# Kernel tuning notes

Hardware: AMD Instinct MI355X
Metric: run time of the kernel (lower is better)

The kernel has to match this reference:

```python
import jax, jax.numpy as jnp
import numpy as np
import math

B, S, D, H = 2, 2048, 1024, 16
DK = D // H

def setup_inputs() -> dict:
    key = jax.random.key(0)
    ks = jax.random.split(key, 12)
    std = 1.0 / math.sqrt(D)
    inp = {
        'query': jax.random.normal(ks[0], (B, S, D), jnp.float32),
        'key':   jax.random.normal(ks[1], (B, S, D), jnp.float32),
        'value': jax.random.normal(ks[2], (B, S, D), jnp.float32),
        'mask':  jnp.ones((B, 1, 1, S), dtype=bool),
        'wq': jax.random.normal(ks[3], (D, D), jnp.float32) * std,
        'bq': jnp.zeros((D,), jnp.float32),
        'wk': jax.random.normal(ks[4], (D, D), jnp.float32) * std,
        'bk': jnp.zeros((D,), jnp.float32),
        'wv': jax.random.normal(ks[5], (D, D), jnp.float32) * std,
        'bv': jnp.zeros((D,), jnp.float32),
        'wo': jax.random.normal(ks[6], (D, D), jnp.float32) * std,
        'bo': jnp.zeros((D,), jnp.float32),
    }
    return inp

def reference(query, key, value, mask, wq, bq, wk, bk, wv, bv, wo, bo):
    # torch.nn.Linear: y = x @ W^T + b
    def split_heads(x):  # [B,S,D] -> [B,H,S,DK]
        return x.reshape(B, -1, H, DK).transpose(0, 2, 1, 3)
    Q = split_heads(query @ wq.T + bq)
    K = split_heads(key @ wk.T + bk)
    V = split_heads(value @ wv.T + bv)
    scale = 1.0 / math.sqrt(DK)
    scores = jnp.einsum('bhtd,bhsd->bhts', Q, K * scale)  # [B,H,S,S]
    scores = jnp.where(mask, scores, -jnp.inf)
    attn = jax.nn.softmax(scores, axis=-1)
    # dropout p=0.0 (eval) -> identity
    context = jnp.einsum('bhts,bhsd->bhtd', attn, V)
    context = context.transpose(0, 2, 1, 3).reshape(B, -1, D)
    return context @ wo.T + bo
```

## Files before the change

kernel.cpp:

```cpp
#include <hip/hip_runtime.h>
#include <stdint.h>

#define SEQ 2048
#define NH  16

typedef __bf16 bf16x8 __attribute__((ext_vector_type(8)));
typedef float  f32x4  __attribute__((ext_vector_type(4)));

#if __has_builtin(__builtin_amdgcn_exp2f)
#define EXP2(x) __builtin_amdgcn_exp2f(x)
#else
#define EXP2(x) exp2f(x)
#endif

__device__ __forceinline__ unsigned short f2bf(float f) {
  union { float f; uint32_t u; } v; v.f = f;
  uint32_t r = v.u + 0x7fffu + ((v.u >> 16) & 1u);
  return (unsigned short)(r >> 16);
}

__device__ __forceinline__ void gll16(const void* g, void* l) {
  __builtin_amdgcn_global_load_lds((const __attribute__((address_space(1))) void*)g,
                                   (__attribute__((address_space(3))) void*)l, 16, 0, 0);
}

__device__ __forceinline__ f32x4 mfma16(bf16x8 a, bf16x8 b, f32x4 c) {
  return __builtin_amdgcn_mfma_f32_16x16x32_bf16(a, b, c, 0, 0, 0);
}

__global__ void cvt_bf16(const float* __restrict__ src, unsigned short* __restrict__ dst, int n4) {
  int i = blockIdx.x * blockDim.x + threadIdx.x;
  int st = gridDim.x * blockDim.x;
  for (; i < n4; i += st) {
    float4 v = ((const float4*)src)[i];
    union { unsigned short u[4]; uint2 q; } o;
    o.u[0] = f2bf(v.x); o.u[1] = f2bf(v.y); o.u[2] = f2bf(v.z); o.u[3] = f2bf(v.w);
    ((uint2*)dst)[i] = o.q;
  }
}

template<int MODE>
__global__ __launch_bounds__(256, 2) void gemm_bt(const unsigned short* __restrict__ A,
                                                  const unsigned short* __restrict__ W,
                                                  const float* __restrict__ bias,
                                                  void* __restrict__ outp, float scale) {
  __shared__ alignas(16) unsigned short Asm[64 * 64];
  __shared__ alignas(16) unsigned short Bsm[128 * 64];
  const int tid = threadIdx.x;
  const int l = tid & 63, w = tid >> 6;
  const int wr = w >> 1, wc = w & 1;
  const int lg = l >> 4, lo = l & 15;
  const int m0 = blockIdx.x * 64, n0 = blockIdx.y * 128;

  f32x4 acc[2][4] = {};

  for (int kt = 0; kt < 16; ++kt) {
    __syncthreads();
#pragma unroll
    for (int it = 0; it < 2; ++it) {
      int chunk = it * 256 + tid;
      int row = chunk >> 3, c = chunk & 7;
      const char* src = (const char*)A + (((size_t)(m0 + row) << 10) + (kt << 6)) * 2 + ((c ^ (row & 7)) << 4);
      gll16(src, (char*)Asm + ((it * 256 + (tid & ~63)) << 4));
    }
#pragma unroll
    for (int it = 0; it < 4; ++it) {
      int chunk = it * 256 + tid;
      int row = chunk >> 3, c = chunk & 7;
      const char* src = (const char*)W + (((size_t)(n0 + row) << 10) + (kt << 6)) * 2 + ((c ^ (row & 7)) << 4);
      gll16(src, (char*)Bsm + ((it * 256 + (tid & ~63)) << 4));
    }
    __syncthreads();
#pragma unroll
    for (int kf = 0; kf < 2; ++kf) {
      bf16x8 af[2], bfr[4];
#pragma unroll
      for (int mf = 0; mf < 2; ++mf) {
        int row = wr * 32 + mf * 16 + lo;
        int pos = (kf * 4 + lg) ^ (row & 7);
        af[mf] = *(const bf16x8*)((const char*)Asm + row * 128 + pos * 16);
      }
#pragma unroll
      for (int nf = 0; nf < 4; ++nf) {
        int row = wc * 64 + nf * 16 + lo;
        int pos = (kf * 4 + lg) ^ (row & 7);
        bfr[nf] = *(const bf16x8*)((const char*)Bsm + row * 128 + pos * 16);
      }
#pragma unroll
      for (int mf = 0; mf < 2; ++mf)
#pragma unroll
        for (int nf = 0; nf < 4; ++nf)
          acc[mf][nf] = mfma16(af[mf], bfr[nf], acc[mf][nf]);
    }
  }
#pragma unroll
  for (int mf = 0; mf < 2; ++mf)
#pragma unroll
    for (int nf = 0; nf < 4; ++nf) {
      int gcol = n0 + wc * 64 + nf * 16 + lo;
      float bv = bias[gcol];
#pragma unroll
      for (int r = 0; r < 4; ++r) {
        int grow = m0 + wr * 32 + mf * 16 + lg * 4 + r;
        float v = (acc[mf][nf][r] + bv) * scale;
        if (MODE == 2) {
          ((float*)outp)[((size_t)grow << 10) + gcol] = v;
        } else {
          int b = grow >> 11, s = grow & 2047, h = gcol >> 6, dk = gcol & 63;
          size_t idx;
          if (MODE == 0) idx = ((((size_t)((b << 4) + h) << 11) + s) << 6) + dk;
          else           idx = ((((size_t)((b << 4) + h) << 6) + dk) << 11) + s;
          ((unsigned short*)outp)[idx] = f2bf(v);
        }
      }
    }
}

__global__ __launch_bounds__(256, 2) void attn_kernel(const unsigned short* __restrict__ Qb,
                                                      const unsigned short* __restrict__ Kb,
                                                      const unsigned short* __restrict__ Vt,
                                                      unsigned short* __restrict__ ctx) {
  __shared__ alignas(16) unsigned short Ksm[64 * 64];
  __shared__ alignas(16) unsigned short Vsm[64 * 64];
  __shared__ alignas(16) unsigned short Psm[4 * 32 * 64];
  const int tid = threadIdx.x;
  const int l = tid & 63, w = tid >> 6;
  const int lg = l >> 4, lo = l & 15;
  const int bh = blockIdx.y;
  const unsigned short* Qp = Qb + (size_t)bh * SEQ * 64;
  const unsigned short* Kp = Kb + (size_t)bh * SEQ * 64;
  const unsigned short* Vp = Vt + (size_t)bh * 64 * SEQ;
  const int q0 = blockIdx.x * 128 + w * 32;

  bf16x8 qf[2][2];
#pragma unroll
  for (int mf = 0; mf < 2; ++mf)
#pragma unroll
    for (int kc = 0; kc < 2; ++kc)
      qf[mf][kc] = *(const bf16x8*)((const char*)Qp + (((size_t)(q0 + mf * 16 + lo)) << 7) + kc * 64 + lg * 16);

  f32x4 O[2][4] = {};
  float m_[2], l_[2];
  m_[0] = m_[1] = -1e30f;
  l_[0] = l_[1] = 0.f;

  for (int t = 0; t < SEQ / 64; ++t) {
    const int kv0 = t << 6;
    __syncthreads();
#pragma unroll
    for (int it = 0; it < 2; ++it) {
      int chunk = it * 256 + tid;
      int row = chunk >> 3, c = chunk & 7;
      const char* ksrc = (const char*)Kp + ((size_t)(kv0 + row) << 7) + ((c ^ (row & 7)) << 4);
      gll16(ksrc, (char*)Ksm + ((it * 256 + (tid & ~63)) << 4));
      const char* vsrc = (const char*)Vp + ((size_t)row << 12) + (kv0 << 1) + ((c ^ (row & 7)) << 4);
      gll16(vsrc, (char*)Vsm + ((it * 256 + (tid & ~63)) << 4));
    }
    __syncthreads();

    f32x4 sfr[4][2] = {};
#pragma unroll
    for (int kc = 0; kc < 2; ++kc) {
      bf16x8 kfr[4];
#pragma unroll
      for (int kvf = 0; kvf < 4; ++kvf) {
        int kv = kvf * 16 + lo;
        int pos = (kc * 4 + lg) ^ (kv & 7);
        kfr[kvf] = *(const bf16x8*)((const char*)Ksm + kv * 128 + pos * 16);
      }
#pragma unroll
      for (int kvf = 0; kvf < 4; ++kvf)
#pragma unroll
        for (int qfi = 0; qfi < 2; ++qfi)
          sfr[kvf][qfi] = mfma16(kfr[kvf], qf[qfi][kc], sfr[kvf][qfi]);
    }

    float tmx[2];
#pragma unroll
    for (int qfi = 0; qfi < 2; ++qfi) {
      float a0 = fmaxf(fmaxf(sfr[0][qfi][0], sfr[0][qfi][1]), fmaxf(sfr[0][qfi][2], sfr[0][qfi][3]));
      float a1 = fmaxf(fmaxf(sfr[1][qfi][0], sfr[1][qfi][1]), fmaxf(sfr[1][qfi][2], sfr[1][qfi][3]));
      float a2 = fmaxf(fmaxf(sfr[2][qfi][0], sfr[2][qfi][1]), fmaxf(sfr[2][qfi][2], sfr[2][qfi][3]));
      float a3 = fmaxf(fmaxf(sfr[3][qfi][0], sfr[3][qfi][1]), fmaxf(sfr[3][qfi][2], sfr[3][qfi][3]));
      float mx = fmaxf(fmaxf(a0, a1), fmaxf(a2, a3));
      mx = fmaxf(mx, __shfl_xor(mx, 16));
      mx = fmaxf(mx, __shfl_xor(mx, 32));
      tmx[qfi] = mx;
    }
    bool need = (tmx[0] > m_[0]) | (tmx[1] > m_[1]);
    if (__any((int)need)) {
      float facv[2];
#pragma unroll
      for (int qfi = 0; qfi < 2; ++qfi) {
        float mnew = fmaxf(m_[qfi], tmx[qfi]);
        facv[qfi] = EXP2(m_[qfi] - mnew);
        m_[qfi] = mnew;
        float ps = 0.f;
#pragma unroll
        for (int kvf = 0; kvf < 4; ++kvf)
#pragma unroll
          for (int r = 0; r < 4; ++r) {
            float p = EXP2(sfr[kvf][qfi][r] - mnew);
            sfr[kvf][qfi][r] = p;
            ps += p;
          }
        ps += __shfl_xor(ps, 16);
        ps += __shfl_xor(ps, 32);
        l_[qfi] = l_[qfi] * facv[qfi] + ps;
      }
#pragma unroll
      for (int mf = 0; mf < 2; ++mf)
#pragma unroll
        for (int r = 0; r < 4; ++r) {
          float fb = __shfl(facv[mf], lg * 4 + r);
#pragma unroll
          for (int dkf = 0; dkf < 4; ++dkf) O[mf][dkf][r] *= fb;
        }
    } else {
#pragma unroll
      for (int qfi = 0; qfi < 2; ++qfi) {
        float ps = 0.f;
#pragma unroll
        for (int kvf = 0; kvf < 4; ++kvf)
#pragma unroll
          for (int r = 0; r < 4; ++r) {
            float p = EXP2(sfr[kvf][qfi][r] - m_[qfi]);
            sfr[kvf][qfi][r] = p;
            ps += p;
          }
        ps += __shfl_xor(ps, 16);
        ps += __shfl_xor(ps, 32);
        l_[qfi] += ps;
      }
    }

#pragma unroll
    for (int qfi = 0; qfi < 2; ++qfi) {
      int ql = qfi * 16 + lo;
      int sw = ql & 7;
#pragma unroll
      for (int kvf = 0; kvf < 4; ++kvf) {
        union { __bf16 b[4]; unsigned long long u; } pk;
#pragma unroll
        for (int r = 0; r < 4; ++r) pk.b[r] = (__bf16)sfr[kvf][qfi][r];
        int g = kvf * 2 + (lg >> 1);
        *(unsigned long long*)((char*)Psm + w * 4096 + ql * 128 + ((g ^ sw) << 4) + ((lg & 1) << 3)) = pk.u;
      }
    }

    bf16x8 af[2][2];
#pragma unroll
    for (int mf = 0; mf < 2; ++mf)
#pragma unroll
      for (int kc = 0; kc < 2; ++kc) {
        int ql = mf * 16 + lo;
        int pos = (kc * 4 + lg) ^ (ql & 7);
        af[mf][kc] = *(const bf16x8*)((const char*)Psm + w * 4096 + ql * 128 + pos * 16);
      }
#pragma unroll
    for (int dkf = 0; dkf < 4; ++dkf) {
      bf16x8 bvf[2];
#pragma unroll
      for (int kc = 0; kc < 2; ++kc) {
        int dk = dkf * 16 + lo;
        int pos = (kc * 4 + lg) ^ (dk & 7);
        bvf[kc] = *(const bf16x8*)((const char*)Vsm + dk * 128 + pos * 16);
      }
#pragma unroll
      for (int mf = 0; mf < 2; ++mf) {
        O[mf][dkf] = mfma16(af[mf][0], bvf[0], O[mf][dkf]);
        O[mf][dkf] = mfma16(af[mf][1], bvf[1], O[mf][dkf]);
      }
    }
  }

  const int b = bh >> 4, h = bh & 15;
#pragma unroll
  for (int mf = 0; mf < 2; ++mf)
#pragma unroll
    for (int r = 0; r < 4; ++r) {
      float lr = __shfl(l_[mf], lg * 4 + r);
      float inv = 1.f / lr;
      int srow = q0 + mf * 16 + lg * 4 + r;
      size_t rowoff = ((size_t)(b * SEQ + srow) << 10) + h * 64;
#pragma unroll
      for (int dkf = 0; dkf < 4; ++dkf)
        ctx[rowoff + dkf * 16 + lo] = f2bf(O[mf][dkf][r] * inv);
    }
}

extern "C" void kernel_launch(void* const* d_in, const int* in_sizes, int n_in,
                              void* d_out, int out_size, void* d_ws, size_t ws_size,
                              hipStream_t stream) {
  const float* query = (const float*)d_in[0];
  const float* key_  = (const float*)d_in[1];
  const float* value = (const float*)d_in[2];
  const float* wq = (const float*)d_in[4];
  const float* bq = (const float*)d_in[5];
  const float* wk = (const float*)d_in[6];
  const float* bk = (const float*)d_in[7];
  const float* wv = (const float*)d_in[8];
  const float* bv = (const float*)d_in[9];
  const float* wo = (const float*)d_in[10];
  const float* bo = (const float*)d_in[11];
  float* out = (float*)d_out;

  char* ws = (char*)d_ws;
  unsigned short* xq  = (unsigned short*)(ws + 0);
  unsigned short* xk  = (unsigned short*)(ws + 8388608);
  unsigned short* xv  = (unsigned short*)(ws + 16777216);
  unsigned short* wqb = (unsigned short*)(ws + 25165824);
  unsigned short* wkb = (unsigned short*)(ws + 27262976);
  unsigned short* wvb = (unsigned short*)(ws + 29360128);
  unsigned short* wob = (unsigned short*)(ws + 31457280);
  unsigned short* Qb  = (unsigned short*)(ws + 33554432);
  unsigned short* Kb  = (unsigned short*)(ws + 41943040);
  unsigned short* Vb  = (unsigned short*)(ws + 50331648);
  unsigned short* ctx = (unsigned short*)(ws + 58720256);

  cvt_bf16<<<1024, 256, 0, stream>>>(query, xq, 1048576);
  cvt_bf16<<<1024, 256, 0, stream>>>(key_,  xk, 1048576);
  cvt_bf16<<<1024, 256, 0, stream>>>(value, xv, 1048576);
  cvt_bf16<<<512, 256, 0, stream>>>(wq, wqb, 262144);
  cvt_bf16<<<512, 256, 0, stream>>>(wk, wkb, 262144);
  cvt_bf16<<<512, 256, 0, stream>>>(wv, wvb, 262144);
  cvt_bf16<<<512, 256, 0, stream>>>(wo, wob, 262144);

  dim3 gg(64, 8);
  const float kscale = 0.125f * 1.44269504088896340736f;
  gemm_bt<0><<<gg, 256, 0, stream>>>(xq, wqb, bq, (void*)Qb, 1.0f);
  gemm_bt<0><<<gg, 256, 0, stream>>>(xk, wkb, bk, (void*)Kb, kscale);
  gemm_bt<1><<<gg, 256, 0, stream>>>(xv, wvb, bv, (void*)Vb, 1.0f);

  attn_kernel<<<dim3(16, 32), 256, 0, stream>>>(Qb, Kb, Vb, ctx);

  gemm_bt<2><<<gg, 256, 0, stream>>>(ctx, wob, bo, (void*)out, 1.0f);
}
```

Before: 157.3 us.

## Batch launches, double-buffer GEMM and attention loads, enlarge GEMM tiles

Merges the seven bf16 conversion launches into one grid and the three QKV projections into one batched GEMM launch. The GEMM moves to 128x128 tiles with a double-buffered LDS pipeline, overlapping the next tile's global-to-LDS copies with current MFMA work through explicit vmcnt waits. The attention kernel gets the same double-buffered K/V staging and a swizzled 1D block order for cache locality. This cuts launch overhead and exposed load latency, but the larger LDS footprint and accumulator register use may lower occupancy.

```diff
diff --git a/kernel.cpp b/kernel.cpp
--- a/kernel.cpp
+++ b/kernel.cpp
@@ -13,6 +13,11 @@
 #define EXP2(x) exp2f(x)
 #endif
 
+#define WAITV0 asm volatile("s_waitcnt vmcnt(0)" ::: "memory")
+#define WAITV4 asm volatile("s_waitcnt vmcnt(4)" ::: "memory")
+#define WAITV8 asm volatile("s_waitcnt vmcnt(8)" ::: "memory")
+#define SBAR() do { __builtin_amdgcn_sched_barrier(0); __builtin_amdgcn_s_barrier(); __builtin_amdgcn_sched_barrier(0); } while (0)
+
 __device__ __forceinline__ unsigned short f2bf(float f) {
   union { float f; uint32_t u; } v; v.f = f;
   uint32_t r = v.u + 0x7fffu + ((v.u >> 16) & 1u);
@@ -28,89 +33,133 @@
   return __builtin_amdgcn_mfma_f32_16x16x32_bf16(a, b, c, 0, 0, 0);
 }
 
-__global__ void cvt_bf16(const float* __restrict__ src, unsigned short* __restrict__ dst, int n4) {
-  int i = blockIdx.x * blockDim.x + threadIdx.x;
+struct CvtJobs {
+  const float* s[7];
+  unsigned short* d[7];
+  int n4[7];
+};
+
+__global__ void cvt_all(CvtJobs J) {
+  int j = blockIdx.y;
+  const float* __restrict__ s = J.s[j];
+  unsigned short* __restrict__ d = J.d[j];
+  int n4 = J.n4[j];
   int st = gridDim.x * blockDim.x;
-  for (; i < n4; i += st) {
-    float4 v = ((const float4*)src)[i];
+  for (int i = blockIdx.x * blockDim.x + threadIdx.x; i < n4; i += st) {
+    float4 v = ((const float4*)s)[i];
     union { unsigned short u[4]; uint2 q; } o;
     o.u[0] = f2bf(v.x); o.u[1] = f2bf(v.y); o.u[2] = f2bf(v.z); o.u[3] = f2bf(v.w);
-    ((uint2*)dst)[i] = o.q;
+    ((uint2*)d)[i] = o.q;
   }
 }
 
-template<int MODE>
-__global__ __launch_bounds__(256, 2) void gemm_bt(const unsigned short* __restrict__ A,
-                                                  const unsigned short* __restrict__ W,
-                                                  const float* __restrict__ bias,
-                                                  void* __restrict__ outp, float scale) {
-  __shared__ alignas(16) unsigned short Asm[64 * 64];
-  __shared__ alignas(16) unsigned short Bsm[128 * 64];
+struct GemmJobs {
+  const unsigned short* A[3];
+  const unsigned short* W[3];
+  const float* bias[3];
+  void* out[3];
+  float scale[3];
+  int mode[3];
+};
+
+__global__ __launch_bounds__(256, 2) void gemm128(GemmJobs J) {
+  __shared__ alignas(16) unsigned short Asm[2][128 * 64];
+  __shared__ alignas(16) unsigned short Bsm[2][128 * 64];
   const int tid = threadIdx.x;
   const int l = tid & 63, w = tid >> 6;
   const int wr = w >> 1, wc = w & 1;
   const int lg = l >> 4, lo = l & 15;
-  const int m0 = blockIdx.x * 64, n0 = blockIdx.y * 128;
-
-  f32x4 acc[2][4] = {};
+
+  const int nwg = gridDim.x;
+  const int id = blockIdx.x;
+  const int swz = (id & 7) * (nwg >> 3) + (id >> 3);
+  const int g = swz >> 8;
+  const int rem = swz & 255;
+  const int m0 = (rem & 31) * 128;
+  const int n0 = (rem >> 5) * 128;
+
+  const unsigned short* __restrict__ A = J.A[g];
+  const unsigned short* __restrict__ W = J.W[g];
+  const float* __restrict__ bias = J.bias[g];
+  const int mode = J.mode[g];
+  const float scale = J.scale[g];
+
+  f32x4 acc[4][4] = {};
+
+#define GSTAGE(b, kt)                                                                   \
+  do {                                                                                  \
+    _Pragma("unroll")                                                                   \
+    for (int it = 0; it < 4; ++it) {                                                    \
+      int chunk = it * 256 + tid;                                                       \
+      int row = chunk >> 3, c = chunk & 7;                                              \
+      const char* src = (const char*)A + (((size_t)(m0 + row) << 10) + ((kt) << 6)) * 2 \
+                        + ((c ^ (row & 7)) << 4);                                       \
+      gll16(src, (char*)Asm[b] + ((it * 256 + (tid & ~63)) << 4));                      \
+    }                                                                                   \
+    _Pragma("unroll")                                                                   \
+    for (int it = 0; it < 4; ++it) {                                                    \
+      int chunk = it * 256 + tid;                                                       \
+      int row = chunk >> 3, c = chunk & 7;                                              \
+      const char* src = (const char*)W + (((size_t)(n0 + row) << 10) + ((kt) << 6)) * 2 \
+                        + ((c ^ (row & 7)) << 4);                                       \
+      gll16(src, (char*)Bsm[b] + ((it * 256 + (tid & ~63)) << 4));                      \
+    }                                                                                   \
+  } while (0)
+
+  GSTAGE(0, 0);
 
   for (int kt = 0; kt < 16; ++kt) {
-    __syncthreads();
-#pragma unroll
-    for (int it = 0; it < 2; ++it) {
-      int chunk = it * 256 + tid;
-      int row = chunk >> 3, c = chunk & 7;
-      const char* src = (const char*)A + (((size_t)(m0 + row) << 10) + (kt << 6)) * 2 + ((c ^ (row & 7)) << 4);
-      gll16(src, (char*)Asm + ((it * 256 + (tid & ~63)) << 4));
-    }
-#pragma unroll
-    for (int it = 0; it < 4; ++it) {
-      int chunk = it * 256 + tid;
-      int row = chunk >> 3, c = chunk & 7;
-      const char* src = (const char*)W + (((size_t)(n0 + row) << 10) + (kt << 6)) * 2 + ((c ^ (row & 7)) << 4);
-      gll16(src, (char*)Bsm + ((it * 256 + (tid & ~63)) << 4));
-    }
-    __syncthreads();
+    const int cur = kt & 1;
+    if (kt < 15) {
+      GSTAGE(cur ^ 1, kt + 1);
+      WAITV8;
+    } else {
+      WAITV0;
+    }
+    SBAR();
 #pragma unroll
     for (int kf = 0; kf < 2; ++kf) {
-      bf16x8 af[2], bfr[4];
-#pragma unroll
-      for (int mf = 0; mf < 2; ++mf) {
-        int row = wr * 32 + mf * 16 + lo;
+      bf16x8 af[4], bfr[4];
+#pragma unroll
+      for (int mf = 0; mf < 4; ++mf) {
+        int row = wr * 64 + mf * 16 + lo;
         int pos = (kf * 4 + lg) ^ (row & 7);
-        af[mf] = *(const bf16x8*)((const char*)Asm + row * 128 + pos * 16);
+        af[mf] = *(const bf16x8*)((const char*)Asm[cur] + row * 128 + pos * 16);
       }
 #pragma unroll
       for (int nf = 0; nf < 4; ++nf) {
         int row = wc * 64 + nf * 16 + lo;
         int pos = (kf * 4 + lg) ^ (row & 7);
-        bfr[nf] = *(const bf16x8*)((const char*)Bsm + row * 128 + pos * 16);
-      }
-#pragma unroll
-      for (int mf = 0; mf < 2; ++mf)
+        bfr[nf] = *(const bf16x8*)((const char*)Bsm[cur] + row * 128 + pos * 16);
+      }
+#pragma unroll
+      for (int mf = 0; mf < 4; ++mf)
 #pragma unroll
         for (int nf = 0; nf < 4; ++nf)
           acc[mf][nf] = mfma16(af[mf], bfr[nf], acc[mf][nf]);
     }
+    SBAR();
   }
-#pragma unroll
-  for (int mf = 0; mf < 2; ++mf)
+#undef GSTAGE
+
+#pragma unroll
+  for (int mf = 0; mf < 4; ++mf)
 #pragma unroll
     for (int nf = 0; nf < 4; ++nf) {
       int gcol = n0 + wc * 64 + nf * 16 + lo;
       float bv = bias[gcol];
 #pragma unroll
       for (int r = 0; r < 4; ++r) {
-        int grow = m0 + wr * 32 + mf * 16 + lg * 4 + r;
+        int grow = m0 + wr * 64 + mf * 16 + lg * 4 + r;
         float v = (acc[mf][nf][r] + bv) * scale;
-        if (MODE == 2) {
-          ((float*)outp)[((size_t)grow << 10) + gcol] = v;
+        if (mode == 2) {
+          ((float*)J.out[g])[((size_t)grow << 10) + gcol] = v;
         } else {
           int b = grow >> 11, s = grow & 2047, h = gcol >> 6, dk = gcol & 63;
           size_t idx;
-          if (MODE == 0) idx = ((((size_t)((b << 4) + h) << 11) + s) << 6) + dk;
+          if (mode == 0) idx = ((((size_t)((b << 4) + h) << 11) + s) << 6) + dk;
           else           idx = ((((size_t)((b << 4) + h) << 6) + dk) << 11) + s;
-          ((unsigned short*)outp)[idx] = f2bf(v);
+          ((__bf16*)J.out[g])[idx] = (__bf16)v;
         }
       }
     }
@@ -120,17 +169,22 @@
                                                       const unsigned short* __restrict__ Kb,
                                                       const unsigned short* __restrict__ Vt,
                                                       unsigned short* __restrict__ ctx) {
-  __shared__ alignas(16) unsigned short Ksm[64 * 64];
-  __shared__ alignas(16) unsigned short Vsm[64 * 64];
+  __shared__ alignas(16) unsigned short Ksm[2][64 * 64];
+  __shared__ alignas(16) unsigned short Vsm[2][64 * 64];
   __shared__ alignas(16) unsigned short Psm[4 * 32 * 64];
   const int tid = threadIdx.x;
   const int l = tid & 63, w = tid >> 6;
   const int lg = l >> 4, lo = l & 15;
-  const int bh = blockIdx.y;
+
+  const int id = blockIdx.x;
+  const int swz = (id & 7) * 64 + (id >> 3);
+  const int bh = swz >> 4;
+  const int qt = swz & 15;
+
   const unsigned short* Qp = Qb + (size_t)bh * SEQ * 64;
   const unsigned short* Kp = Kb + (size_t)bh * SEQ * 64;
   const unsigned short* Vp = Vt + (size_t)bh * 64 * SEQ;
-  const int q0 = blockIdx.x * 128 + w * 32;
+  const int q0 = qt * 128 + w * 32;
 
   bf16x8 qf[2][2];
 #pragma unroll
@@ -138,25 +192,38 @@
 #pragma unroll
     for (int kc = 0; kc < 2; ++kc)
       qf[mf][kc] = *(const bf16x8*)((const char*)Qp + (((size_t)(q0 + mf * 16 + lo)) << 7) + kc * 64 + lg * 16);
+  WAITV0;
 
   f32x4 O[2][4] = {};
   float m_[2], l_[2];
   m_[0] = m_[1] = -1e30f;
   l_[0] = l_[1] = 0.f;
 
+#define ASTAGE(b, t)                                                                      \
+  do {                                                                                    \
+    const int kv0s = (t) << 6;                                                            \
+    _Pragma("unroll")                                                                     \
+    for (int it = 0; it < 2; ++it) {                                                      \
+      int chunk = it * 256 + tid;                                                         \
+      int row = chunk >> 3, c = chunk & 7;                                                \
+      const char* ksrc = (const char*)Kp + ((size_t)(kv0s + row) << 7) + ((c ^ (row & 7)) << 4); \
+      gll16(ksrc, (char*)Ksm[b] + ((it * 256 + (tid & ~63)) << 4));                       \
+      const char* vsrc = (const char*)Vp + ((size_t)row << 12) + (kv0s << 1) + ((c ^ (row & 7)) << 4); \
+      gll16(vsrc, (char*)Vsm[b] + ((it * 256 + (tid & ~63)) << 4));                       \
+    }                                                                                     \
+  } while (0)
+
+  ASTAGE(0, 0);
+
   for (int t = 0; t < SEQ / 64; ++t) {
-    const int kv0 = t << 6;
-    __syncthreads();
-#pragma unroll
-    for (int it = 0; it < 2; ++it) {
-      int chunk = it * 256 + tid;
-      int row = chunk >> 3, c = chunk & 7;
-      const char* ksrc = (const char*)Kp + ((size_t)(kv0 + row) << 7) + ((c ^ (row & 7)) << 4);
-      gll16(ksrc, (char*)Ksm + ((it * 256 + (tid & ~63)) << 4));
-      const char* vsrc = (const char*)Vp + ((size_t)row << 12) + (kv0 << 1) + ((c ^ (row & 7)) << 4);
-      gll16(vsrc, (char*)Vsm + ((it * 256 + (tid & ~63)) << 4));
-    }
-    __syncthreads();
+    const int cur = t & 1;
+    if (t < SEQ / 64 - 1) {
+      ASTAGE(cur ^ 1, t + 1);
+      WAITV4;
+    } else {
+      WAITV0;
+    }
+    SBAR();
 
     f32x4 sfr[4][2] = {};
 #pragma unroll
@@ -166,7 +233,7 @@
       for (int kvf = 0; kvf < 4; ++kvf) {
         int kv = kvf * 16 + lo;
         int pos = (kc * 4 + lg) ^ (kv & 7);
-        kfr[kvf] = *(const bf16x8*)((const char*)Ksm + kv * 128 + pos * 16);
+        kfr[kvf] = *(const bf16x8*)((const char*)Ksm[cur] + kv * 128 + pos * 16);
       }
 #pragma unroll
       for (int kvf = 0; kvf < 4; ++kvf)
@@ -264,7 +331,7 @@
       for (int kc = 0; kc < 2; ++kc) {
         int dk = dkf * 16 + lo;
         int pos = (kc * 4 + lg) ^ (dk & 7);
-        bvf[kc] = *(const bf16x8*)((const char*)Vsm + dk * 128 + pos * 16);
+        bvf[kc] = *(const bf16x8*)((const char*)Vsm[cur] + dk * 128 + pos * 16);
       }
 #pragma unroll
       for (int mf = 0; mf < 2; ++mf) {
@@ -272,7 +339,9 @@
         O[mf][dkf] = mfma16(af[mf][1], bvf[1], O[mf][dkf]);
       }
     }
+    SBAR();
   }
+#undef ASTAGE
 
   const int b = bh >> 4, h = bh & 15;
 #pragma unroll
@@ -285,7 +354,7 @@
       size_t rowoff = ((size_t)(b * SEQ + srow) << 10) + h * 64;
 #pragma unroll
       for (int dkf = 0; dkf < 4; ++dkf)
-        ctx[rowoff + dkf * 16 + lo] = f2bf(O[mf][dkf][r] * inv);
+        ((__bf16*)ctx)[rowoff + dkf * 16 + lo] = (__bf16)(O[mf][dkf][r] * inv);
     }
 }
 
@@ -303,7 +372,6 @@
   const float* bv = (const float*)d_in[9];
   const float* wo = (const float*)d_in[10];
   const float* bo = (const float*)d_in[11];
-  float* out = (float*)d_out;
 
   char* ws = (char*)d_ws;
   unsigned short* xq  = (unsigned short*)(ws + 0);
@@ -318,21 +386,28 @@
   unsigned short* Vb  = (unsigned short*)(ws + 50331648);
   unsigned short* ctx = (unsigned short*)(ws + 58720256);
 
-  cvt_bf16<<<1024, 256, 0, stream>>>(query, xq, 1048576);
-  cvt_bf16<<<1024, 256, 0, stream>>>(key_,  xk, 1048576);
-  cvt_bf16<<<1024, 256, 0, stream>>>(value, xv, 1048576);
-  cvt_bf16<<<512, 256, 0, stream>>>(wq, wqb, 262144);
-  cvt_bf16<<<512, 256, 0, stream>>>(wk, wkb, 262144);
-  cvt_bf16<<<512, 256, 0, stream>>>(wv, wvb, 262144);
-  cvt_bf16<<<512, 256, 0, stream>>>(wo, wob, 262144);
-
-  dim3 gg(64, 8);
+  CvtJobs cj;
+  cj.s[0] = query; cj.d[0] = xq;  cj.n4[0] = 1048576;
+  cj.s[1] = key_;  cj.d[1] = xk;  cj.n4[1] = 1048576;
+  cj.s[2] = value; cj.d[2] = xv;  cj.n4[2] = 1048576;
+  cj.s[3] = wq;    cj.d[3] = wqb; cj.n4[3] = 262144;
+  cj.s[4] = wk;    cj.d[4] = wkb; cj.n4[4] = 262144;
+  cj.s[5] = wv;    cj.d[5] = wvb; cj.n4[5] = 262144;
+  cj.s[6] = wo;    cj.d[6] = wob; cj.n4[6] = 262144;
+  cvt_all<<<dim3(256, 7), 256, 0, stream>>>(cj);
+
   const float kscale = 0.125f * 1.44269504088896340736f;
-  gemm_bt<0><<<gg, 256, 0, stream>>>(xq, wqb, bq, (void*)Qb, 1.0f);
-  gemm_bt<0><<<gg, 256, 0, stream>>>(xk, wkb, bk, (void*)Kb, kscale);
-  gemm_bt<1><<<gg, 256, 0, stream>>>(xv, wvb, bv, (void*)Vb, 1.0f);
-
-  attn_kernel<<<dim3(16, 32), 256, 0, stream>>>(Qb, Kb, Vb, ctx);
-
-  gemm_bt<2><<<gg, 256, 0, stream>>>(ctx, wob, bo, (void*)out, 1.0f);
-}
+  GemmJobs gj;
+  gj.A[0] = xq; gj.W[0] = wqb; gj.bias[0] = bq; gj.out[0] = (void*)Qb; gj.scale[0] = 1.0f;   gj.mode[0] = 0;
+  gj.A[1] = xk; gj.W[1] = wkb; gj.bias[1] = bk; gj.out[1] = (void*)Kb; gj.scale[1] = kscale; gj.mode[1] = 0;
+  gj.A[2] = xv; gj.W[2] = wvb; gj.bias[2] = bv; gj.out[2] = (void*)Vb; gj.scale[2] = 1.0f;   gj.mode[2] = 1;
+  gemm128<<<768, 256, 0, stream>>>(gj);
+
+  attn_kernel<<<512, 256, 0, stream>>>(Qb, Kb, Vb, ctx);
+
+  GemmJobs oj;
+  oj.A[0] = ctx; oj.W[0] = wob; oj.bias[0] = bo; oj.out[0] = d_out; oj.scale[0] = 1.0f; oj.mode[0] = 2;
+  oj.A[1] = oj.A[0]; oj.W[1] = oj.W[0]; oj.bias[1] = oj.bias[0]; oj.out[1] = oj.out[0]; oj.scale[1] = 1.0f; oj.mode[1] = 2;
+  oj.A[2] = oj.A[0]; oj.W[2] = oj.W[0]; oj.bias[2] = oj.bias[0]; oj.out[2] = oj.out[0]; oj.scale[2] = 1.0f; oj.mode[2] = 2;
+  gemm128<<<256, 256, 0, stream>>>(oj);
+}
```

After: 167.7 us. +6.6%, slower.
